# Optimization experiments

Hardware: AMD Instinct MI355X
Metric: run time of the kernel (lower is better)

Reference implementation:

```python
import jax, jax.numpy as jnp
import numpy as np

H, W = 512, 1024
R = 5                      # circle_radius
K = 2 * R + 1              # circle_k_size = 11
NMS_K = 7                  # nms_kernel_size
TOP_K = 200

# static circle geometry (matches registered buffers)
_ky, _kx = np.mgrid[0:K, 0:K]
OFF_X = (_kx + 1 - (K + 1) // 2).astype(np.float32)  # circle_coords[0]
OFF_Y = (_ky + 1 - (K + 1) // 2).astype(np.float32)  # circle_coords[1]
_circle_dists = np.sqrt(OFF_X ** 2 + OFF_Y ** 2)
CIRCLE_MASK = (_circle_dists <= R).astype(np.float32)
N_CIRCLE = float(CIRCLE_MASK.sum())
CENTER_THRESH = float((_circle_dists * CIRCLE_MASK).sum() / N_CIRCLE + 0.5)


def setup_inputs() -> dict:
    key = jax.random.key(0)
    k1, k2 = jax.random.split(key)
    fg_pred = jax.random.uniform(k1, (1, 1, H, W), dtype=jnp.float32)
    center_regressions = jax.random.normal(k2, (1, 2, H, W), dtype=jnp.float32)
    return {"fg_pred": fg_pred, "center_regressions": center_regressions}


def _vote_map(center_regressions):
    """Circular-mask Hough voting error + 1, shape (B, H, W)."""
    B = center_regressions.shape[0]
    pad = K // 2
    rp = jnp.pad(center_regressions, ((0, 0), (0, 0), (pad, pad), (pad, pad)))
    err = jnp.zeros((B, H, W), jnp.float32)
    # loop over fixed 11x11 kernel taps (only the ~81 inside the circle)
    for iy in range(K):
        for ix in range(K):
            if CIRCLE_MASK[iy, ix] == 0.0:
                continue
            rx = rp[:, 0, iy:iy + H, ix:ix + W]
            ry = rp[:, 1, iy:iy + H, ix:ix + W]
            err = err + jnp.sqrt((OFF_X[iy, ix] - rx) ** 2 + (OFF_Y[iy, ix] - ry) ** 2)
    return err / N_CIRCLE + 1.0


def reference(fg_pred, center_regressions):
    B = fg_pred.shape[0]
    xs_grid = jnp.arange(1, W + 1, dtype=jnp.float32)[None, :]
    ys_grid = jnp.arange(1, H + 1, dtype=jnp.float32)[:, None]
    pred_x = xs_grid - center_regressions[:, 0]  # (B, H, W)
    pred_y = ys_grid - center_regressions[:, 1]
    things = fg_pred[:, 0] >= 0.5                # (B, H, W)

    vote = _vote_map(center_regressions)
    # NMS: -maxpool(-x) == minpool, torch pads with -inf for maxpool -> +inf here
    hp = NMS_K // 2
    pooled = jax.lax.reduce_window(vote, jnp.inf, jax.lax.min,
                                   (1, NMS_K, NMS_K), (1, 1, 1),
                                   [(0, 0), (hp, hp), (hp, hp)])
    vote = jnp.where(pooled == vote, vote, 0.0)
    vote = jnp.where(vote >= CENTER_THRESH, 0.0, vote)

    # get_centers: top_k smallest nonzero errors (padded with +inf / valid mask)
    flat = vote.reshape(B, H * W)
    cand = jnp.where(flat > 0.0, flat, jnp.inf)
    neg_err, idx = jax.lax.top_k(-cand, TOP_K)   # smallest errors, ascending
    cerr = -neg_err                              # (B, TOP_K)
    valid = jnp.isfinite(cerr)
    cy = (idx // W).astype(jnp.float32)          # 0-based rows (torch.nonzero)
    cx = (idx % W).astype(jnp.float32)

    # create_inst_maps: assign each pixel to nearest center (argmin over K centers)
    dist2 = (pred_x[..., None] - cx[:, None, None, :]) ** 2 + \
            (pred_y[..., None] - cy[:, None, None, :]) ** 2  # (B, H, W, TOP_K)
    dist2 = jnp.where(valid[:, None, None, :], dist2, jnp.inf)
    inst = jnp.argmin(dist2, axis=-1).astype(jnp.int32) + 1
    any_valid = valid.any(axis=1)
    inst = inst * things.astype(jnp.int32) * any_valid[:, None, None].astype(jnp.int32)

    coords = jnp.stack([cy, cx], axis=-1).astype(jnp.int32)  # (B, TOP_K, 2) as (y, x)
    cerr_out = jnp.where(valid, cerr, 0.0)
    return inst, coords, cerr_out
```

## Files before the change

kernel.cpp:

```cpp
#include <hip/hip_runtime.h>
#include <math.h>

#define HH 512
#define WW 1024
#define RR 5
#define KK 11
#define TOPK 200
#define MAXC 16384

#define BW 64
#define BH 16
#define TT 4
#define SROWS (BH + 10)
#define SCOLS (BW + 10)


__global__ __launch_bounds__(256) void vote_kernel(const float* __restrict__ cr,
                                                   float* __restrict__ vote,
                                                   int* __restrict__ meta) {
    __shared__ float2 s[SROWS][SCOLS + 2];
    const int tid = threadIdx.x;
    const int bx = blockIdx.x * BW, by = blockIdx.y * BH;

    if (bx == 0 && by == 0 && tid < 4) meta[tid] = 0;

    for (int l = tid; l < SROWS * SCOLS; l += 256) {
        int r = l / SCOLS, c = l % SCOLS;
        int gy = by - 5 + r, gx = bx - 5 + c;
        bool ok = (gy >= 0) && (gy < HH) && (gx >= 0) && (gx < WW);
        float vx = ok ? cr[gy * WW + gx] : 0.0f;
        float vy = ok ? cr[HH * WW + gy * WW + gx] : 0.0f;
        s[r][c] = make_float2(vx, vy);
    }
    __syncthreads();

    const int x = tid & 63;
    const int yt = tid >> 6;
    float a[TT] = {0.f, 0.f, 0.f, 0.f};
    float b[TT] = {0.f, 0.f, 0.f, 0.f};

    #pragma unroll
    for (int rr = 0; rr < TT + 10; ++rr) {
        #pragma unroll
        for (int ix = 0; ix < KK; ++ix) {
            const int ox = ix - 5;
            bool any = false;
            #pragma unroll
            for (int t = 0; t < TT; ++t) {
                const int oy = rr - 5 - t;
                if (oy >= -RR && oy <= RR && ox * ox + oy * oy <= RR * RR) any = true;
            }
            if (!any) continue;
            float2 v = s[yt * TT + rr][x + ix];
            #pragma unroll
            for (int t = 0; t < TT; ++t) {
                const int oy = rr - 5 - t;
                if (oy >= -RR && oy <= RR && ox * ox + oy * oy <= RR * RR) {
                    float dx = (float)ox - v.x;
                    float dy = (float)oy - v.y;
                    float sv = __builtin_amdgcn_sqrtf(fmaf(dy, dy, dx * dx));
                    if (ix & 1) b[t] += sv; else a[t] += sv;
                }
            }
        }
    }
    const int y0 = by + yt * TT;
    #pragma unroll
    for (int t = 0; t < TT; ++t)
        vote[(y0 + t) * WW + bx + x] = (a[t] + b[t]) / 81.0f + 1.0f;
}

__global__ __launch_bounds__(256) void nms_kernel(const float* __restrict__ vote,
                                                  float* __restrict__ cv, int* __restrict__ ci,
                                                  int* __restrict__ meta, float ct) {
    const int tid = threadIdx.x;
    const int x = blockIdx.x * 64 + (tid & 63);
    const int y0 = blockIdx.y * 16 + (tid >> 6) * 4;

    int xc[7];
    #pragma unroll
    for (int d = 0; d < 7; ++d) xc[d] = min(max(x + d - 3, 0), WW - 1);

    float r[10], c[4];
    #pragma unroll
    for (int j = 0; j < 10; ++j) {
        int yy = min(max(y0 + j - 3, 0), HH - 1);
        const float* row = vote + yy * WW;
        float m0 = fminf(row[xc[0]], row[xc[1]]);
        float m1 = fminf(row[xc[2]], row[xc[3]]);
        float m2 = fminf(row[xc[4]], row[xc[5]]);
        float m3 = row[xc[6]];
        if (j >= 3 && j < 7) c[j - 3] = row[xc[3]];
        r[j] = fminf(fminf(m0, m1), fminf(m2, m3));
    }
    float p[9], q4[7];
    #pragma unroll
    for (int j = 0; j < 9; ++j) p[j] = fminf(r[j], r[j + 1]);
    #pragma unroll
    for (int j = 0; j < 7; ++j) q4[j] = fminf(p[j], p[j + 2]);
    #pragma unroll
    for (int t = 0; t < 4; ++t) {
        float m = fminf(q4[t], q4[t + 3]);
        float v = c[t];
        if (v == m && v < ct) {
            int s = atomicAdd(&meta[0], 1);
            if (s < MAXC) { cv[s] = v; ci[s] = (y0 + t) * WW + x; }
        }
    }
}

__global__ __launch_bounds__(256) void select_kernel(const float* __restrict__ cv,
                                                     const int* __restrict__ ci,
                                                     int* __restrict__ meta,
                                                     float* __restrict__ selx,
                                                     float* __restrict__ sely,
                                                     float* __restrict__ out) {
    __shared__ float bv[256];
    __shared__ int bi[256];
    __shared__ int s_idx[TOPK];
    __shared__ float s_val[TOPK];
    const int tid = threadIdx.x;
    int M = meta[0];
    if (M > MAXC) M = MAXC;
    const int Mtop = (M < TOPK) ? M : TOPK;

    float lastv = -INFINITY;
    int lasti = -1;
    for (int k = 0; k < Mtop; ++k) {
        float bestv = INFINITY;
        int besti = 0x7fffffff;
        for (int j = tid; j < M; j += 256) {
            float cvj = cv[j];
            int cij = ci[j];
            if (cvj > lastv || (cvj == lastv && cij > lasti)) {
                if (cvj < bestv || (cvj == bestv && cij < besti)) { bestv = cvj; besti = cij; }
            }
        }
        bv[tid] = bestv; bi[tid] = besti;
        __syncthreads();
        for (int s = 128; s > 0; s >>= 1) {
            if (tid < s) {
                float ov = bv[tid + s]; int oi = bi[tid + s];
                if (ov < bv[tid] || (ov == bv[tid] && oi < bi[tid])) { bv[tid] = ov; bi[tid] = oi; }
            }
            __syncthreads();
        }
        lastv = bv[0]; lasti = bi[0];
        if (tid == 0) { s_val[k] = lastv; s_idx[k] = lasti; }
        __syncthreads();
    }

    for (int k = Mtop + tid; k < TOPK; k += 256) {
        int r = k - Mtop;
        int g = r, prev = -1;
        while (g != prev) {
            prev = g;
            int cnt = 0;
            for (int j = 0; j < M; ++j) cnt += (ci[j] <= g) ? 1 : 0;
            g = r + cnt;
        }
        s_idx[k] = g;
        s_val[k] = INFINITY;
    }
    if (tid == 0) {
        meta[1] = Mtop;
        meta[2] = (M > 0) ? 1 : 0;
    }
    __syncthreads();

    for (int k = tid; k < TOPK; k += 256) {
        int idx = s_idx[k];
        int cy = idx >> 10;
        int cx = idx & (WW - 1);
        out[HH * WW + 2 * k]     = (float)cy;
        out[HH * WW + 2 * k + 1] = (float)cx;
        bool valid = (k < Mtop);
        out[HH * WW + 2 * TOPK + k] = valid ? s_val[k] : 0.0f;
        selx[k] = (float)cx;
        sely[k] = (float)cy;
    }
}

__global__ __launch_bounds__(256) void inst_kernel(const float* __restrict__ fg,
                                                   const float* __restrict__ cr,
                                                   const float* __restrict__ selx,
                                                   const float* __restrict__ sely,
                                                   const int* __restrict__ meta,
                                                   float* __restrict__ out) {
    int idx4 = blockIdx.x * 256 + threadIdx.x;
    const int Mtop = meta[1];
    const int anyv = meta[2];
    float4 o = make_float4(0.f, 0.f, 0.f, 0.f);
    if (anyv) {
        int pix0 = idx4 * 4;
        int y = pix0 >> 10;
        float4 f = ((const float4*)fg)[idx4];
        float4 cx0 = ((const float4*)cr)[idx4];
        float4 cy0 = ((const float4*)(cr + HH * WW))[idx4];
        float fgv[4] = {f.x, f.y, f.z, f.w};
        float crx[4] = {cx0.x, cx0.y, cx0.z, cx0.w};
        float cry[4] = {cy0.x, cy0.y, cy0.z, cy0.w};
        float res[4];
        #pragma unroll
        for (int t = 0; t < 4; ++t) {
            res[t] = 0.f;
            if (fgv[t] >= 0.5f) {
                int x = (pix0 + t) & (WW - 1);
                float px = (float)(x + 1) - crx[t];
                float py = (float)(y + 1) - cry[t];
                float best = INFINITY;
                int bk = 0;
                for (int k = 0; k < Mtop; ++k) {
                    float ddx = px - selx[k];
                    float ddy = py - sely[k];
                    float d = ddx * ddx + ddy * ddy;
                    if (d < best) { best = d; bk = k; }
                }
                res[t] = (float)(bk + 1);
            }
        }
        o = make_float4(res[0], res[1], res[2], res[3]);
    }
    ((float4*)out)[idx4] = o;
}

extern "C" void kernel_launch(void* const* d_in, const int* in_sizes, int n_in,
                              void* d_out, int out_size, void* d_ws, size_t ws_size,
                              hipStream_t stream) {
    const float* fg = (const float*)d_in[0];
    const float* cr = (const float*)d_in[1];
    float* out = (float*)d_out;

    char* ws = (char*)d_ws;
    int* meta = (int*)ws;
    float* vote = (float*)(ws + 64);
    float* cv = (float*)(ws + 64 + 4 * HH * WW);
    int* ci = (int*)(ws + 64 + 4 * HH * WW + 4 * MAXC);
    float* selx = (float*)(ws + 64 + 4 * HH * WW + 8 * MAXC);
    float* sely = selx + TOPK;

    double s = 0.0;
    int n = 0;
    for (int iy = 0; iy < KK; ++iy)
        for (int ix = 0; ix < KK; ++ix) {
            double dx = ix - RR, dy = iy - RR;
            double d = sqrt(dx * dx + dy * dy);
            if (d <= (double)RR) { s += d; n++; }
        }
    float ct = (float)(s / n + 0.5);

    dim3 vgrid(WW / BW, HH / BH);
    vote_kernel<<<vgrid, 256, 0, stream>>>(cr, vote, meta);
    dim3 ngrid(WW / 64, HH / 16);
    nms_kernel<<<ngrid, 256, 0, stream>>>(vote, cv, ci, meta, ct);
    select_kernel<<<1, 256, 0, stream>>>(cv, ci, meta, selx, sely, out);
    inst_kernel<<<(HH * WW / 4) / 256, 256, 0, stream>>>(fg, cr, selx, sely, meta, out);
}
```

Baseline: 23.72 us.

## Fuse top-k selection into instance kernel, recomputing selection in every block

Merges the single-block select kernel into the instance-assignment kernel: each of the 512 blocks redundantly runs the top-k selection over the candidate list and keeps the chosen centers in shared memory. Block 0 writes the coords and errors output. This removes one kernel launch and the global round-trip for the selected centers, and the distance loop now reads centers from LDS. The cost is that the serial selection, up to 200 block reductions over all candidates, is repeated in every block, which adds a lot of redundant work when many candidates exist.

```diff
diff --git a/kernel.cpp b/kernel.cpp
--- a/kernel.cpp
+++ b/kernel.cpp
@@ -109,16 +109,18 @@
     }
 }
 
-__global__ __launch_bounds__(256) void select_kernel(const float* __restrict__ cv,
-                                                     const int* __restrict__ ci,
-                                                     int* __restrict__ meta,
-                                                     float* __restrict__ selx,
-                                                     float* __restrict__ sely,
-                                                     float* __restrict__ out) {
+__global__ __launch_bounds__(256) void inst_select_kernel(const float* __restrict__ fg,
+                                                          const float* __restrict__ cr,
+                                                          const float* __restrict__ cv,
+                                                          const int* __restrict__ ci,
+                                                          const int* __restrict__ meta,
+                                                          float* __restrict__ out) {
     __shared__ float bv[256];
     __shared__ int bi[256];
     __shared__ int s_idx[TOPK];
     __shared__ float s_val[TOPK];
+    __shared__ float s_selx[TOPK];
+    __shared__ float s_sely[TOPK];
     const int tid = threadIdx.x;
     int M = meta[0];
     if (M > MAXC) M = MAXC;
@@ -162,36 +164,26 @@
         s_idx[k] = g;
         s_val[k] = INFINITY;
     }
-    if (tid == 0) {
-        meta[1] = Mtop;
-        meta[2] = (M > 0) ? 1 : 0;
-    }
     __syncthreads();
 
     for (int k = tid; k < TOPK; k += 256) {
         int idx = s_idx[k];
-        int cy = idx >> 10;
-        int cx = idx & (WW - 1);
-        out[HH * WW + 2 * k]     = (float)cy;
-        out[HH * WW + 2 * k + 1] = (float)cx;
-        bool valid = (k < Mtop);
-        out[HH * WW + 2 * TOPK + k] = valid ? s_val[k] : 0.0f;
-        selx[k] = (float)cx;
-        sely[k] = (float)cy;
-    }
-}
-
-__global__ __launch_bounds__(256) void inst_kernel(const float* __restrict__ fg,
-                                                   const float* __restrict__ cr,
-                                                   const float* __restrict__ selx,
-                                                   const float* __restrict__ sely,
-                                                   const int* __restrict__ meta,
-                                                   float* __restrict__ out) {
-    int idx4 = blockIdx.x * 256 + threadIdx.x;
-    const int Mtop = meta[1];
-    const int anyv = meta[2];
+        s_sely[k] = (float)(idx >> 10);
+        s_selx[k] = (float)(idx & (WW - 1));
+    }
+    __syncthreads();
+
+    if (blockIdx.x == 0) {
+        for (int k = tid; k < TOPK; k += 256) {
+            out[HH * WW + 2 * k]     = s_sely[k];
+            out[HH * WW + 2 * k + 1] = s_selx[k];
+            out[HH * WW + 2 * TOPK + k] = (k < Mtop) ? s_val[k] : 0.0f;
+        }
+    }
+
+    int idx4 = blockIdx.x * 256 + tid;
     float4 o = make_float4(0.f, 0.f, 0.f, 0.f);
-    if (anyv) {
+    if (M > 0) {
         int pix0 = idx4 * 4;
         int y = pix0 >> 10;
         float4 f = ((const float4*)fg)[idx4];
@@ -211,8 +203,8 @@
                 float best = INFINITY;
                 int bk = 0;
                 for (int k = 0; k < Mtop; ++k) {
-                    float ddx = px - selx[k];
-                    float ddy = py - sely[k];
+                    float ddx = px - s_selx[k];
+                    float ddy = py - s_sely[k];
                     float d = ddx * ddx + ddy * ddy;
                     if (d < best) { best = d; bk = k; }
                 }
@@ -236,8 +228,6 @@
     float* vote = (float*)(ws + 64);
     float* cv = (float*)(ws + 64 + 4 * HH * WW);
     int* ci = (int*)(ws + 64 + 4 * HH * WW + 4 * MAXC);
-    float* selx = (float*)(ws + 64 + 4 * HH * WW + 8 * MAXC);
-    float* sely = selx + TOPK;
 
     double s = 0.0;
     int n = 0;
@@ -253,6 +243,5 @@
     vote_kernel<<<vgrid, 256, 0, stream>>>(cr, vote, meta);
     dim3 ngrid(WW / 64, HH / 16);
     nms_kernel<<<ngrid, 256, 0, stream>>>(vote, cv, ci, meta, ct);
-    select_kernel<<<1, 256, 0, stream>>>(cv, ci, meta, selx, sely, out);
-    inst_kernel<<<(HH * WW / 4) / 256, 256, 0, stream>>>(fg, cr, selx, sely, meta, out);
-}
+    inst_select_kernel<<<(HH * WW / 4) / 256, 256, 0, stream>>>(fg, cr, cv, ci, meta, out);
+}
```

New measurement: 22.47 us. 5.3% less time.
